# Optimization experiments

Measured on AMD Instinct MI355X. Metric: run time of the kernel, lower is better.

The kernel has to match this reference:

```python
import jax, jax.numpy as jnp
import numpy as np

D_MODEL = 1024
E_MODEL = 2
D_STATE = 16
D_CONV = 4
D_IN = E_MODEL * D_MODEL            # 2048
DT_RANK = int(np.ceil(D_MODEL / 16))  # 64
B_SZ, SEQ = 1, 2048


def setup_inputs() -> dict:
    key = jax.random.key(0)
    ks = jax.random.split(key, 9)
    s = lambda fan: 1.0 / np.sqrt(fan)
    return {
        "x": jax.random.normal(ks[0], (B_SZ, SEQ, D_MODEL), jnp.float32),
        "W_in": jax.random.normal(ks[1], (D_MODEL, 2 * D_IN), jnp.float32) * s(D_MODEL),
        "conv_w": jax.random.normal(ks[2], (D_CONV, D_IN), jnp.float32) * s(D_CONV),
        "conv_b": jnp.zeros((D_IN,), jnp.float32),
        "W_x": jax.random.normal(ks[3], (D_IN, DT_RANK + 2 * D_STATE), jnp.float32) * s(D_IN),
        "W_dt": jax.random.normal(ks[4], (DT_RANK, D_IN), jnp.float32) * s(DT_RANK),
        "b_dt": jax.random.normal(ks[5], (D_IN,), jnp.float32) * 0.01,
        "D": jnp.ones((D_IN,), jnp.float32),
        "W_out": jax.random.normal(ks[6], (D_IN, D_MODEL), jnp.float32) * s(D_IN),
    }


def _causal_depthwise_conv(x, w, b):
    # x: (b, l, d_in); w: (d_conv, d_in) depthwise taps; causal left pad
    L = x.shape[1]
    xp = jnp.pad(x, ((0, 0), (D_CONV - 1, 0), (0, 0)))
    y = b
    for k in range(D_CONV):  # small fixed kernel width
        y = y + xp[:, k:k + L, :] * w[k]
    return y


def _selective_scan(u, delta, A, Bm, Cm, D):
    # u, delta: (b,l,d); A: (d,n); Bm, Cm: (b,l,n); D: (d,)
    dA = jnp.einsum('bld,dn->bldn', delta, A)
    dB_u = jnp.einsum('bld,bld,bln->bldn', delta, u, Bm)
    # replicate tf.pad(dA[:,1:], [[0,0],[1,1],[0,0],[0,0]])[:,1:]
    t = jnp.pad(dA[:, 1:], ((0, 0), (1, 1), (0, 0), (0, 0)))[:, 1:]
    t = jnp.flip(t, axis=1)
    t = jnp.cumsum(t, axis=1)
    dA_cs = jnp.flip(jnp.exp(t), axis=1)
    xs = jnp.cumsum(dB_u * dA_cs, axis=1) / (dA_cs + 1e-12)
    y = jnp.einsum('bldn,bln->bld', xs, Cm)
    return y + u * D


def reference(x, W_in, conv_w, conv_b, W_x, W_dt, b_dt, D, W_out):
    seq_len = x.shape[1]
    x_and_res = x @ W_in                                  # (b,l,2*d_in)
    xi, res = jnp.split(x_and_res, [D_IN], axis=-1)
    xi = _causal_depthwise_conv(xi, conv_w, conv_b)[:, :seq_len, :]
    xi = jax.nn.swish(xi)
    # SSM
    A = -jnp.exp(jnp.log(jnp.arange(1, D_STATE + 1, dtype=jnp.float32)))  # (n,)
    A = jnp.broadcast_to(A, (D_IN, D_STATE))
    x_dbl = xi @ W_x                                      # (b,l,dtr+2n)
    delta, Bm, Cm = jnp.split(x_dbl, [DT_RANK, DT_RANK + D_STATE], axis=-1)
    delta = jax.nn.softplus(delta @ W_dt + b_dt)          # (b,l,d_in)
    y = _selective_scan(xi, delta, A, Bm, Cm, D)
    y = y * jax.nn.swish(res)
    return y @ W_out
```

## Files before the change

### kernel.cpp

```cpp
#include <hip/hip_runtime.h>
#include <hip/hip_bf16.h>

#define L_SEQ 2048
#define DMODEL 1024
#define DIN 2048
#define DTR 64
#define NST 16
#define CCH 128
#define CHL 16

typedef unsigned short u16;
typedef __bf16 bf16x8 __attribute__((ext_vector_type(8)));
typedef float f32x4 __attribute__((ext_vector_type(4)));

__device__ inline u16 f2bf(float v) {
    __bf16 h = (__bf16)v;
    return __builtin_bit_cast(unsigned short, h);
}
__device__ inline float rcpf(float x) { return __builtin_amdgcn_rcpf(x); }
__device__ inline float swishf(float v) { return v * rcpf(1.f + __expf(-v)); }
__device__ inline float softplusf(float v) {
    return (v > 20.f) ? v : __logf(1.f + __expf(v));
}

__device__ inline void powers16(float v, float* p) {
    p[0] = v;
    p[1] = v * v;
    p[2] = p[1] * v;
    p[3] = p[1] * p[1];
    p[4] = p[3] * p[0];  p[5] = p[3] * p[1];  p[6] = p[3] * p[2];  p[7] = p[3] * p[3];
    p[8] = p[7] * p[0];  p[9] = p[7] * p[1];  p[10] = p[7] * p[2]; p[11] = p[7] * p[3];
    p[12] = p[7] * p[4]; p[13] = p[7] * p[5]; p[14] = p[7] * p[6]; p[15] = p[7] * p[7];
}

template<int TBN, bool SP>
__global__ __launch_bounds__(256) void gemm_bf16(const u16* __restrict__ A,
                                                 const u16* __restrict__ Bt,
                                                 float* __restrict__ C,
                                                 const float* __restrict__ bias,
                                                 int M, int N, int K) {
    constexpr int LDSZ = (128 + TBN) * 64;
    constexpr int ROUNDS = (128 + TBN) / 32;
    constexpr int FN = TBN / 32;
    __shared__ u16 smem[2 * LDSZ];

    const int tid = threadIdx.x;
    const int lane = tid & 63;
    const int wid = tid >> 6;
    const int wm = wid >> 1;
    const int wn = wid & 1;
    const int bm = blockIdx.y * 128;
    const int bn = blockIdx.x * TBN;

    const int srow8 = lane >> 3;
    const int schunk = lane & 7;
    const int lm = lane & 15;
    const int lk = lane >> 4;

    f32x4 acc[4][FN];
#pragma unroll
    for (int i = 0; i < 4; ++i)
#pragma unroll
        for (int j = 0; j < FN; ++j) acc[i][j] = (f32x4){0.f, 0.f, 0.f, 0.f};

    auto stage = [&](int buf, int t) {
        const int k0 = t * 64;
        u16* base = smem + buf * LDSZ;
#pragma unroll
        for (int rr = 0; rr < ROUNDS; ++rr) {
            int row = rr * 32 + wid * 8;
            int grow = row + srow8;
            const u16* src;
            if (row < 128) src = A + (size_t)(bm + grow) * K + k0 + schunk * 8;
            else           src = Bt + (size_t)(bn + grow - 128) * K + k0 + schunk * 8;
            u16* dst = base + row * 64;
            __builtin_amdgcn_global_load_lds(
                (const __attribute__((address_space(1))) void*)src,
                (__attribute__((address_space(3))) void*)dst, 16, 0, 0);
        }
    };

    auto compute = [&](int buf) {
        const u16* base = smem + buf * LDSZ;
#pragma unroll
        for (int kk = 0; kk < 2; ++kk) {
            bf16x8 av[4], bv[FN];
#pragma unroll
            for (int fm = 0; fm < 4; ++fm)
                av[fm] = *(const bf16x8*)(base + (wm * 64 + fm * 16 + lm) * 64 + kk * 32 + lk * 8);
#pragma unroll
            for (int fn = 0; fn < FN; ++fn)
                bv[fn] = *(const bf16x8*)(base + (128 + wn * (TBN / 2) + fn * 16 + lm) * 64 + kk * 32 + lk * 8);
#pragma unroll
            for (int fm = 0; fm < 4; ++fm)
#pragma unroll
                for (int fn = 0; fn < FN; ++fn)
                    acc[fm][fn] = __builtin_amdgcn_mfma_f32_16x16x32_bf16(av[fm], bv[fn], acc[fm][fn], 0, 0, 0);
        }
    };

    const int nt = K / 64;
    int cur = 0;
    stage(0, 0);
    __syncthreads();
    for (int t = 0; t < nt - 1; ++t) {
        stage(cur ^ 1, t + 1);
        compute(cur);
        __syncthreads();
        cur ^= 1;
    }
    compute(cur);

#pragma unroll
    for (int fm = 0; fm < 4; ++fm) {
#pragma unroll
        for (int fn = 0; fn < FN; ++fn) {
            int col = bn + wn * (TBN / 2) + fn * 16 + lm;
#pragma unroll
            for (int j = 0; j < 4; ++j) {
                int row = bm + wm * 64 + fm * 16 + lk * 4 + j;
                float v = acc[fm][fn][j];
                if (SP) {
                    v += bias[col];
                    v = softplusf(v);
                }
                C[(size_t)row * N + col] = v;
            }
        }
    }
}

__global__ __launch_bounds__(256) void gemm_bf16_sk(const u16* __restrict__ A, int lda,
                                                    const u16* __restrict__ Bt, int ldb,
                                                    float* __restrict__ P,
                                                    int M, int N, int K, int kc) {
    constexpr int TBN = 32;
    constexpr int LDSZ = (128 + TBN) * 64;
    constexpr int ROUNDS = (128 + TBN) / 32;
    __shared__ u16 smem[2 * LDSZ];

    const int tid = threadIdx.x;
    const int lane = tid & 63;
    const int wid = tid >> 6;
    const int wm = wid >> 1;
    const int wn = wid & 1;
    const int bm = blockIdx.y * 128;
    const int bn = blockIdx.x * TBN;
    const int kbeg = blockIdx.z * kc;
    float* Cz = P + (size_t)blockIdx.z * M * N;

    const int srow8 = lane >> 3;
    const int schunk = lane & 7;
    const int lm = lane & 15;
    const int lk = lane >> 4;

    f32x4 acc[4];
#pragma unroll
    for (int i = 0; i < 4; ++i) acc[i] = (f32x4){0.f, 0.f, 0.f, 0.f};

    auto stage = [&](int buf, int t) {
        const int k0 = kbeg + t * 64;
        u16* base = smem + buf * LDSZ;
#pragma unroll
        for (int rr = 0; rr < ROUNDS; ++rr) {
            int row = rr * 32 + wid * 8;
            int grow = row + srow8;
            const u16* src;
            if (row < 128) src = A + (size_t)(bm + grow) * lda + k0 + schunk * 8;
            else           src = Bt + (size_t)(bn + grow - 128) * ldb + k0 + schunk * 8;
            u16* dst = base + row * 64;
            __builtin_amdgcn_global_load_lds(
                (const __attribute__((address_space(1))) void*)src,
                (__attribute__((address_space(3))) void*)dst, 16, 0, 0);
        }
    };

    auto compute = [&](int buf) {
        const u16* base = smem + buf * LDSZ;
#pragma unroll
        for (int kk = 0; kk < 2; ++kk) {
            bf16x8 av[4], bv;
#pragma unroll
            for (int fm = 0; fm < 4; ++fm)
                av[fm] = *(const bf16x8*)(base + (wm * 64 + fm * 16 + lm) * 64 + kk * 32 + lk * 8);
            bv = *(const bf16x8*)(base + (128 + wn * 16 + lm) * 64 + kk * 32 + lk * 8);
#pragma unroll
            for (int fm = 0; fm < 4; ++fm)
                acc[fm] = __builtin_amdgcn_mfma_f32_16x16x32_bf16(av[fm], bv, acc[fm], 0, 0, 0);
        }
    };

    const int nt = kc / 64;
    int cur = 0;
    stage(0, 0);
    __syncthreads();
    for (int t = 0; t < nt - 1; ++t) {
        stage(cur ^ 1, t + 1);
        compute(cur);
        __syncthreads();
        cur ^= 1;
    }
    compute(cur);

#pragma unroll
    for (int fm = 0; fm < 4; ++fm) {
        int col = bn + wn * 16 + lm;
#pragma unroll
        for (int j = 0; j < 4; ++j) {
            int row = bm + wm * 64 + fm * 16 + lk * 4 + j;
            Cz[(size_t)row * N + col] = acc[fm][j];
        }
    }
}

__device__ inline void castT_dev(const float* __restrict__ W, u16* __restrict__ Wt,
                                 int K, int N, int bx, int by) {
    __shared__ u16 tile[64][65];
    int n0 = bx * 64, k0 = by * 64;
    int tn = threadIdx.x & 63, t4 = threadIdx.x >> 6;
#pragma unroll
    for (int j = 0; j < 16; ++j) {
        int k = t4 + j * 4;
        if (n0 + tn < N) tile[tn][k] = f2bf(W[(size_t)(k0 + k) * N + n0 + tn]);
    }
    __syncthreads();
#pragma unroll
    for (int j = 0; j < 16; ++j) {
        int n = t4 + j * 4;
        if (n0 + n < N) Wt[(size_t)(n0 + n) * K + k0 + tn] = tile[n][tn];
    }
}

__global__ __launch_bounds__(256) void prep_fused(const float* __restrict__ x,
                                                  const float* __restrict__ W_in,
                                                  const float* __restrict__ W_x,
                                                  const float* __restrict__ W_dt,
                                                  const float* __restrict__ W_out,
                                                  u16* __restrict__ xbf,
                                                  u16* __restrict__ WinT,
                                                  u16* __restrict__ WxT,
                                                  u16* __restrict__ WdtT,
                                                  u16* __restrict__ WoutT) {
    int b = blockIdx.x;
    if (b < 2048) {
        int i = b * 256 + threadIdx.x;
        float4 v = ((const float4*)x)[i];
        ushort4 o;
        o.x = f2bf(v.x); o.y = f2bf(v.y); o.z = f2bf(v.z); o.w = f2bf(v.w);
        ((ushort4*)xbf)[i] = o;
    } else if (b < 3072) {
        int t = b - 2048;
        castT_dev(W_in, WinT, DMODEL, 4096, t & 63, t >> 6);
    } else if (b < 3136) {
        int t = b - 3072;
        castT_dev(W_x, WxT, DIN, 96, t & 1, t >> 1);
    } else if (b < 3168) {
        int t = b - 3136;
        castT_dev(W_dt, WdtT, DTR, DIN, t, 0);
    } else {
        int t = b - 3168;
        castT_dev(W_out, WoutT, DIN, DMODEL, t & 15, t >> 4);
    }
}

__global__ __launch_bounds__(256) void reduce_sk(const float* __restrict__ P,
                                                 float* __restrict__ xdbl,
                                                 u16* __restrict__ xdbf) {
    int i = blockIdx.x * 256 + threadIdx.x;
    float s = 0.f;
#pragma unroll
    for (int z = 0; z < 8; ++z) s += P[z * (L_SEQ * 96) + i];
    xdbl[i] = s;
    int l = i / 96, k = i - l * 96;
    if (k < DTR) xdbf[l * DTR + k] = f2bf(s);
}

__global__ __launch_bounds__(256) void conv_swish(const float* __restrict__ xr,
                                                  const float* __restrict__ cw,
                                                  const float* __restrict__ cb,
                                                  float* __restrict__ xi,
                                                  u16* __restrict__ xib) {
    int id = blockIdx.x * 256 + threadIdx.x;
    int l = id >> 11;
    int d = id & (DIN - 1);
    float acc = cb[d];
#pragma unroll
    for (int k = 0; k < 4; ++k) {
        int ls = l - 3 + k;
        if (ls >= 0) acc += xr[ls * 4096 + d] * cw[k * DIN + d];
    }
    float sw = swishf(acc);
    xi[id] = sw;
    xib[id] = f2bf(sw);
}

__global__ __launch_bounds__(256) void scanA(const float* __restrict__ delta,
                                             const float* __restrict__ u,
                                             const float* __restrict__ xdbl,
                                             float* __restrict__ localQ,
                                             float* __restrict__ csum) {
    __shared__ float sh[CHL][16];
    const int tid = threadIdx.x;
    const int c = blockIdx.y;
    const int d = blockIdx.x * 256 + tid;
    const int l0 = c * CHL;
    {
        int l = tid >> 4, j = tid & 15;
        sh[l][j] = xdbl[(l0 + l) * 96 + DTR + j];
    }
    __syncthreads();
    float q[16];
#pragma unroll
    for (int n = 0; n < 16; ++n) q[n] = 0.f;
    float s = 0.f;
#pragma unroll 2
    for (int l = 0; l < CHL; ++l) {
        float dl = delta[(l0 + l) * DIN + d];
        float ul = u[(l0 + l) * DIN + d];
        float bb[16];
        const float4* shv = (const float4*)&sh[l][0];
        *(float4*)&bb[0] = shv[0];  *(float4*)&bb[4] = shv[1];
        *(float4*)&bb[8] = shv[2];  *(float4*)&bb[12] = shv[3];
        float v = __expf(-dl);
        float p[16];
        powers16(v, p);
        float dlul = dl * ul;
#pragma unroll
        for (int n = 0; n < 16; ++n) q[n] = q[n] * p[n] + dlul * bb[n];
        s += dl;
    }
    float* dst = localQ + (size_t)(c * DIN + d) * 16;
    *(float4*)(dst + 0)  = make_float4(q[0], q[1], q[2], q[3]);
    *(float4*)(dst + 4)  = make_float4(q[4], q[5], q[6], q[7]);
    *(float4*)(dst + 8)  = make_float4(q[8], q[9], q[10], q[11]);
    *(float4*)(dst + 12) = make_float4(q[12], q[13], q[14], q[15]);
    csum[c * DIN + d] = s;
}

__global__ __launch_bounds__(256) void scanB(float* __restrict__ localQ,
                                             const float* __restrict__ csum,
                                             float* __restrict__ send) {
    int gid = blockIdx.x * 256 + threadIdx.x;
    int n = gid & 15;
    int d = gid >> 4;
    const float An = -(float)(n + 1);
    float q = 0.f;
#pragma unroll 4
    for (int c = 0; c < CCH; ++c) {
        float cs = csum[c * DIN + d];
        float w = __expf(An * cs);
        float* lq = localQ + (size_t)(c * DIN + d) * 16 + n;
        float lv = *lq;
        *lq = q;
        q = q * w + lv;
    }
    if (n == 0) {
        double ssum = 0.0;
        for (int c = CCH - 1; c >= 0; --c) {
            ssum += (double)csum[c * DIN + d];
            send[c * DIN + d] = (float)ssum;
        }
    }
}

__global__ __launch_bounds__(256) void scanC(const float* __restrict__ delta,
                                             const float* __restrict__ u,
                                             const float* __restrict__ xdbl,
                                             const float* __restrict__ localQ,
                                             const float* __restrict__ send,
                                             const float* __restrict__ Dvec,
                                             const float* __restrict__ xr,
                                             u16* __restrict__ ybf) {
    __shared__ float sh[CHL][32];
    const int tid = threadIdx.x;
    const int c = blockIdx.y;
    const int d = blockIdx.x * 256 + tid;
    const int l0 = c * CHL;
#pragma unroll
    for (int k = 0; k < 2; ++k) {
        int idx = tid + k * 256;
        int l = idx >> 5, j = idx & 31;
        sh[l][j] = xdbl[(l0 + l) * 96 + DTR + j];
    }
    __syncthreads();
    float q[16];
    {
        const float* src = localQ + (size_t)(c * DIN + d) * 16;
        float4 t0 = *(const float4*)(src + 0);
        float4 t1 = *(const float4*)(src + 4);
        float4 t2 = *(const float4*)(src + 8);
        float4 t3 = *(const float4*)(src + 12);
        q[0] = t0.x; q[1] = t0.y; q[2] = t0.z; q[3] = t0.w;
        q[4] = t1.x; q[5] = t1.y; q[6] = t1.z; q[7] = t1.w;
        q[8] = t2.x; q[9] = t2.y; q[10] = t2.z; q[11] = t2.w;
        q[12] = t3.x; q[13] = t3.y; q[14] = t3.z; q[15] = t3.w;
    }
    const float send_cd = send[c * DIN + d];
    const float Dd = Dvec[d];
    float s = 0.f;
#pragma unroll 2
    for (int l = 0; l < CHL; ++l) {
        float dl = delta[(l0 + l) * DIN + d];
        float ul = u[(l0 + l) * DIN + d];
        float bb[32];
        const float4* shv = (const float4*)&sh[l][0];
        *(float4*)&bb[0]  = shv[0]; *(float4*)&bb[4]  = shv[1];
        *(float4*)&bb[8]  = shv[2]; *(float4*)&bb[12] = shv[3];
        *(float4*)&bb[16] = shv[4]; *(float4*)&bb[20] = shv[5];
        *(float4*)&bb[24] = shv[6]; *(float4*)&bb[28] = shv[7];
        float v = __expf(-dl);
        float p[16];
        powers16(v, p);
        float dlul = dl * ul;
#pragma unroll
        for (int n = 0; n < 16; ++n) q[n] = q[n] * p[n] + dlul * bb[n];
        s += dl;
        float suf = send_cd - s;
        float contrib;
        float ac[4] = {0.f, 0.f, 0.f, 0.f};
        if (suf < 0.8f) {
#pragma unroll
            for (int n = 0; n < 16; ++n) ac[n & 3] += q[n] * bb[16 + n];
            contrib = (ac[0] + ac[1]) + (ac[2] + ac[3]);
        } else {
            float w = __expf(-suf);
            float e[16];
            powers16(w, e);
            if (suf > 40.f) {
#pragma unroll
                for (int n = 0; n < 16; ++n) ac[n & 3] += (q[n] * e[n]) * bb[16 + n];
                contrib = ((ac[0] + ac[1]) + (ac[2] + ac[3])) * 1e12f;
            } else {
#pragma unroll
                for (int n = 0; n < 16; ++n) {
                    float g = e[n] * rcpf(e[n] + 1e-12f);
                    ac[n & 3] += (q[n] * g) * bb[16 + n];
                }
                contrib = (ac[0] + ac[1]) + (ac[2] + ac[3]);
            }
        }
        float y = contrib + ul * Dd;
        float r = xr[(l0 + l) * 4096 + DIN + d];
        ybf[(l0 + l) * DIN + d] = f2bf(y * swishf(r));
    }
}

extern "C" void kernel_launch(void* const* d_in, const int* in_sizes, int n_in,
                              void* d_out, int out_size, void* d_ws, size_t ws_size,
                              hipStream_t stream) {
    const float* x      = (const float*)d_in[0];
    const float* W_in   = (const float*)d_in[1];
    const float* conv_w = (const float*)d_in[2];
    const float* conv_b = (const float*)d_in[3];
    const float* W_x    = (const float*)d_in[4];
    const float* W_dt   = (const float*)d_in[5];
    const float* b_dt   = (const float*)d_in[6];
    const float* Dvec   = (const float*)d_in[7];
    const float* W_out  = (const float*)d_in[8];
    float* out = (float*)d_out;

    float* ws = (float*)d_ws;
    float* xr     = ws;
    float* xi     = ws + 8388608;
    u16*   xibf   = (u16*)(ws + 12582912);
    float* xdbl   = ws + 14680064;
    float* delta  = ws + 14876672;
    float* localQ = ws + 19070976;
    float* csum   = ws + 23265280;
    float* send   = ws + 23527424;
    u16*   xbf    = (u16*)(ws + 23789568);
    u16*   WinT   = (u16*)(ws + 24838144);
    u16*   WxT    = (u16*)(ws + 26935296);
    u16*   WdtT   = (u16*)(ws + 27033600);
    u16*   WoutT  = (u16*)(ws + 27099136);
    u16*   xdbf   = (u16*)(ws + 28147712);
    float* Psk    = ws + 28213248;
    u16*   ybf    = (u16*)(ws + 29786112);

    prep_fused<<<3680, 256, 0, stream>>>(x, W_in, W_x, W_dt, W_out,
                                         xbf, WinT, WxT, WdtT, WoutT);
    gemm_bf16<128, false><<<dim3(4096 / 128, L_SEQ / 128), 256, 0, stream>>>(
        xbf, WinT, xr, nullptr, L_SEQ, 4096, DMODEL);
    conv_swish<<<(L_SEQ * DIN) / 256, 256, 0, stream>>>(xr, conv_w, conv_b, xi, xibf);
    gemm_bf16_sk<<<dim3(3, L_SEQ / 128, 8), 256, 0, stream>>>(
        xibf, DIN, WxT, DIN, Psk, L_SEQ, 96, DIN, 256);
    reduce_sk<<<(L_SEQ * 96) / 256, 256, 0, stream>>>(Psk, xdbl, xdbf);
    gemm_bf16<128, true><<<dim3(DIN / 128, L_SEQ / 128), 256, 0, stream>>>(
        xdbf, WdtT, delta, b_dt, L_SEQ, DIN, DTR);
    scanA<<<dim3(DIN / 256, CCH), 256, 0, stream>>>(delta, xi, xdbl, localQ, csum);
    scanB<<<(DIN * NST) / 256, 256, 0, stream>>>(localQ, csum, send);
    scanC<<<dim3(DIN / 256, CCH), 256, 0, stream>>>(delta, xi, xdbl, localQ, send,
                                                    Dvec, xr, ybf);
    gemm_bf16<64, false><<<dim3(DMODEL / 64, L_SEQ / 128), 256, 0, stream>>>(
        ybf, WoutT, out, nullptr, L_SEQ, DMODEL, DIN);
}
```

Baseline: 162.5 us.

## Split in-proj epilogue into bf16 conv input and precomputed swish gate

The input-projection GEMM epilogue now writes the conv branch as bf16 and the residual branch already passed through swish, replacing the full fp32 projection buffer. Conv and both scan kernels read the bf16 activations instead of a separate fp32 copy of xi, and scanC reads the precomputed gate instead of recomputing swish from the strided fp32 buffer. The split-K for the x_proj GEMM drops from 8 to 4 slices, halving the partial-sum traffic in the reduction. Storing the pre-conv activation and u in bf16 adds rounding error to the scan inputs.

```diff
diff --git a/kernel.cpp b/kernel.cpp
--- a/kernel.cpp
+++ b/kernel.cpp
@@ -16,6 +16,10 @@
 __device__ inline u16 f2bf(float v) {
     __bf16 h = (__bf16)v;
     return __builtin_bit_cast(unsigned short, h);
+}
+__device__ inline float bf2f(u16 v) {
+    __bf16 h = __builtin_bit_cast(__bf16, v);
+    return (float)h;
 }
 __device__ inline float rcpf(float x) { return __builtin_amdgcn_rcpf(x); }
 __device__ inline float swishf(float v) { return v * rcpf(1.f + __expf(-v)); }
@@ -33,11 +37,13 @@
     p[12] = p[7] * p[4]; p[13] = p[7] * p[5]; p[14] = p[7] * p[6]; p[15] = p[7] * p[7];
 }
 
-template<int TBN, bool SP>
+template<int TBN, int EPI>
 __global__ __launch_bounds__(256) void gemm_bf16(const u16* __restrict__ A,
                                                  const u16* __restrict__ Bt,
                                                  float* __restrict__ C,
                                                  const float* __restrict__ bias,
+                                                 u16* __restrict__ xiraw,
+                                                 float* __restrict__ gate,
                                                  int M, int N, int K) {
     constexpr int LDSZ = (128 + TBN) * 64;
     constexpr int ROUNDS = (128 + TBN) / 32;
@@ -120,11 +126,15 @@
             for (int j = 0; j < 4; ++j) {
                 int row = bm + wm * 64 + fm * 16 + lk * 4 + j;
                 float v = acc[fm][fn][j];
-                if (SP) {
+                if (EPI == 0) {
+                    C[(size_t)row * N + col] = v;
+                } else if (EPI == 1) {
                     v += bias[col];
-                    v = softplusf(v);
+                    C[(size_t)row * N + col] = softplusf(v);
+                } else {
+                    if (col < DIN) xiraw[(size_t)row * DIN + col] = f2bf(v);
+                    else           gate[(size_t)row * DIN + (col - DIN)] = swishf(v);
                 }
-                C[(size_t)row * N + col] = v;
             }
         }
     }
@@ -269,16 +279,15 @@
     int i = blockIdx.x * 256 + threadIdx.x;
     float s = 0.f;
 #pragma unroll
-    for (int z = 0; z < 8; ++z) s += P[z * (L_SEQ * 96) + i];
+    for (int z = 0; z < 4; ++z) s += P[z * (L_SEQ * 96) + i];
     xdbl[i] = s;
     int l = i / 96, k = i - l * 96;
     if (k < DTR) xdbf[l * DTR + k] = f2bf(s);
 }
 
-__global__ __launch_bounds__(256) void conv_swish(const float* __restrict__ xr,
+__global__ __launch_bounds__(256) void conv_swish(const u16* __restrict__ xiraw,
                                                   const float* __restrict__ cw,
                                                   const float* __restrict__ cb,
-                                                  float* __restrict__ xi,
                                                   u16* __restrict__ xib) {
     int id = blockIdx.x * 256 + threadIdx.x;
     int l = id >> 11;
@@ -287,15 +296,13 @@
 #pragma unroll
     for (int k = 0; k < 4; ++k) {
         int ls = l - 3 + k;
-        if (ls >= 0) acc += xr[ls * 4096 + d] * cw[k * DIN + d];
-    }
-    float sw = swishf(acc);
-    xi[id] = sw;
-    xib[id] = f2bf(sw);
+        if (ls >= 0) acc += bf2f(xiraw[ls * DIN + d]) * cw[k * DIN + d];
+    }
+    xib[id] = f2bf(swishf(acc));
 }
 
 __global__ __launch_bounds__(256) void scanA(const float* __restrict__ delta,
-                                             const float* __restrict__ u,
+                                             const u16* __restrict__ u,
                                              const float* __restrict__ xdbl,
                                              float* __restrict__ localQ,
                                              float* __restrict__ csum) {
@@ -316,7 +323,7 @@
 #pragma unroll 2
     for (int l = 0; l < CHL; ++l) {
         float dl = delta[(l0 + l) * DIN + d];
-        float ul = u[(l0 + l) * DIN + d];
+        float ul = bf2f(u[(l0 + l) * DIN + d]);
         float bb[16];
         const float4* shv = (const float4*)&sh[l][0];
         *(float4*)&bb[0] = shv[0];  *(float4*)&bb[4] = shv[1];
@@ -364,12 +371,12 @@
 }
 
 __global__ __launch_bounds__(256) void scanC(const float* __restrict__ delta,
-                                             const float* __restrict__ u,
+                                             const u16* __restrict__ u,
                                              const float* __restrict__ xdbl,
                                              const float* __restrict__ localQ,
                                              const float* __restrict__ send,
                                              const float* __restrict__ Dvec,
-                                             const float* __restrict__ xr,
+                                             const float* __restrict__ gate,
                                              u16* __restrict__ ybf) {
     __shared__ float sh[CHL][32];
     const int tid = threadIdx.x;
@@ -401,7 +408,7 @@
 #pragma unroll 2
     for (int l = 0; l < CHL; ++l) {
         float dl = delta[(l0 + l) * DIN + d];
-        float ul = u[(l0 + l) * DIN + d];
+        float ul = bf2f(u[(l0 + l) * DIN + d]);
         float bb[32];
         const float4* shv = (const float4*)&sh[l][0];
         *(float4*)&bb[0]  = shv[0]; *(float4*)&bb[4]  = shv[1];
@@ -440,8 +447,7 @@
             }
         }
         float y = contrib + ul * Dd;
-        float r = xr[(l0 + l) * 4096 + DIN + d];
-        ybf[(l0 + l) * DIN + d] = f2bf(y * swishf(r));
+        ybf[(l0 + l) * DIN + d] = f2bf(y * gate[(l0 + l) * DIN + d]);
     }
 }
 
@@ -460,37 +466,37 @@
     float* out = (float*)d_out;
 
     float* ws = (float*)d_ws;
-    float* xr     = ws;
-    float* xi     = ws + 8388608;
-    u16*   xibf   = (u16*)(ws + 12582912);
-    float* xdbl   = ws + 14680064;
-    float* delta  = ws + 14876672;
-    float* localQ = ws + 19070976;
-    float* csum   = ws + 23265280;
-    float* send   = ws + 23527424;
-    u16*   xbf    = (u16*)(ws + 23789568);
-    u16*   WinT   = (u16*)(ws + 24838144);
-    u16*   WxT    = (u16*)(ws + 26935296);
-    u16*   WdtT   = (u16*)(ws + 27033600);
-    u16*   WoutT  = (u16*)(ws + 27099136);
-    u16*   xdbf   = (u16*)(ws + 28147712);
-    float* Psk    = ws + 28213248;
-    u16*   ybf    = (u16*)(ws + 29786112);
+    u16*   xiraw  = (u16*)ws;
+    float* gate   = ws + 2097152;
+    u16*   xibf   = (u16*)(ws + 6291456);
+    float* xdbl   = ws + 8388608;
+    float* delta  = ws + 8585216;
+    float* localQ = ws + 12779520;
+    float* csum   = ws + 16973824;
+    float* send   = ws + 17235968;
+    u16*   xbf    = (u16*)(ws + 17498112);
+    u16*   WinT   = (u16*)(ws + 18546688);
+    u16*   WxT    = (u16*)(ws + 20643840);
+    u16*   WdtT   = (u16*)(ws + 20742144);
+    u16*   WoutT  = (u16*)(ws + 20807680);
+    u16*   xdbf   = (u16*)(ws + 21856256);
+    float* Psk    = ws + 21921792;
+    u16*   ybf    = (u16*)(ws + 22708224);
 
     prep_fused<<<3680, 256, 0, stream>>>(x, W_in, W_x, W_dt, W_out,
                                          xbf, WinT, WxT, WdtT, WoutT);
-    gemm_bf16<128, false><<<dim3(4096 / 128, L_SEQ / 128), 256, 0, stream>>>(
-        xbf, WinT, xr, nullptr, L_SEQ, 4096, DMODEL);
-    conv_swish<<<(L_SEQ * DIN) / 256, 256, 0, stream>>>(xr, conv_w, conv_b, xi, xibf);
-    gemm_bf16_sk<<<dim3(3, L_SEQ / 128, 8), 256, 0, stream>>>(
-        xibf, DIN, WxT, DIN, Psk, L_SEQ, 96, DIN, 256);
+    gemm_bf16<128, 2><<<dim3(4096 / 128, L_SEQ / 128), 256, 0, stream>>>(
+        xbf, WinT, nullptr, nullptr, xiraw, gate, L_SEQ, 4096, DMODEL);
+    conv_swish<<<(L_SEQ * DIN) / 256, 256, 0, stream>>>(xiraw, conv_w, conv_b, xibf);
+    gemm_bf16_sk<<<dim3(3, L_SEQ / 128, 4), 256, 0, stream>>>(
+        xibf, DIN, WxT, DIN, Psk, L_SEQ, 96, DIN, 512);
     reduce_sk<<<(L_SEQ * 96) / 256, 256, 0, stream>>>(Psk, xdbl, xdbf);
-    gemm_bf16<128, true><<<dim3(DIN / 128, L_SEQ / 128), 256, 0, stream>>>(
-        xdbf, WdtT, delta, b_dt, L_SEQ, DIN, DTR);
-    scanA<<<dim3(DIN / 256, CCH), 256, 0, stream>>>(delta, xi, xdbl, localQ, csum);
+    gemm_bf16<128, 1><<<dim3(DIN / 128, L_SEQ / 128), 256, 0, stream>>>(
+        xdbf, WdtT, delta, b_dt, nullptr, nullptr, L_SEQ, DIN, DTR);
+    scanA<<<dim3(DIN / 256, CCH), 256, 0, stream>>>(delta, xibf, xdbl, localQ, csum);
     scanB<<<(DIN * NST) / 256, 256, 0, stream>>>(localQ, csum, send);
-    scanC<<<dim3(DIN / 256, CCH), 256, 0, stream>>>(delta, xi, xdbl, localQ, send,
-                                                    Dvec, xr, ybf);
-    gemm_bf16<64, false><<<dim3(DMODEL / 64, L_SEQ / 128), 256, 0, stream>>>(
-        ybf, WoutT, out, nullptr, L_SEQ, DMODEL, DIN);
-}
+    scanC<<<dim3(DIN / 256, CCH), 256, 0, stream>>>(delta, xibf, xdbl, localQ, send,
+                                                    Dvec, gate, ybf);
+    gemm_bf16<64, 0><<<dim3(DMODEL / 64, L_SEQ / 128), 256, 0, stream>>>(
+        ybf, WoutT, out, nullptr, nullptr, nullptr, L_SEQ, DMODEL, DIN);
+}
```

Result: no change. 162.9 us (+0.2%).
